# Performance work log

Hardware: AMD Instinct MI355X
Metric: run time of the kernel (lower is better)

## Reference

```python
import jax, jax.numpy as jnp
import numpy as np

B, T, C, H = 4, 4096, 1024, 64

def setup_inputs() -> dict:
    key = jax.random.key(0)
    k1, k2, k3, k4, k5 = jax.random.split(key, 5)
    scale = 0.02
    return {
        "x": jax.random.normal(k1, (B, T, C), dtype=jnp.float32),
        "head_bias": jax.random.normal(k2, (T, T), dtype=jnp.float32) * 0.1,
        "w_k": jax.random.normal(k3, (C, H), dtype=jnp.float32) * scale,
        "w_q": jax.random.normal(k4, (C, H), dtype=jnp.float32) * scale,
        "w_v": jax.random.normal(k5, (C, H), dtype=jnp.float32) * scale,
    }

def reference(x, head_bias, w_k, w_q, w_v):
    # x: (B,T,C) ; projections: (B,T,H)
    k = jnp.einsum('btc,ch->bth', x, w_k)
    q = jnp.einsum('btc,ch->bth', x, w_q)
    v = jnp.einsum('btc,ch->bth', x, w_v)
    Tq = x.shape[1]
    # scores: (B,T,T) with RPE bias and causal mask
    scores = jnp.einsum('bqh,bkh->bqk', q, k) * (k.shape[-1] ** -0.5)
    scores = scores + head_bias[None, :, :]
    causal = jnp.tril(jnp.ones((Tq, Tq), dtype=bool))
    scores = jnp.where(causal[None, :, :], scores, -jnp.inf)
    weights = jax.nn.softmax(scores, axis=-1)
    out = jnp.einsum('bqk,bkh->bqh', weights, v)
    return out
```

## Files before the change

kernel.cpp:

```cpp
#include <hip/hip_runtime.h>
#include <hip/hip_bf16.h>


#define T_DIM 4096
#define C_DIM 1024
#define CK    256

typedef __attribute__((ext_vector_type(8))) short s16x8;
typedef __attribute__((ext_vector_type(4))) float f32x4;
typedef __attribute__((ext_vector_type(2))) unsigned int u32x2;
typedef __attribute__((ext_vector_type(4))) unsigned int u32x4;

__device__ __forceinline__ short f2bf(float f) {
    unsigned u = __builtin_bit_cast(unsigned, f);
    u += 0x7FFFu + ((u >> 16) & 1u);
    return (short)(u >> 16);
}
__device__ __forceinline__ unsigned pack2(float a, float b) {
    unsigned ua = __builtin_bit_cast(unsigned, a);
    unsigned ub = __builtin_bit_cast(unsigned, b);
    ua += 0x7FFFu + ((ua >> 16) & 1u);
    ub += 0x7FFFu + ((ub >> 16) & 1u);
    return __builtin_amdgcn_perm(ub, ua, 0x07060302u);
}
__device__ __forceinline__ float bf2f(short s) {
    unsigned u = ((unsigned)(unsigned short)s) << 16;
    return __builtin_bit_cast(float, u);
}
__device__ __forceinline__ int chunk_off(int qt) {
    int g = qt >> 4, r = qt & 15;
    return qt + 8 * g * (g - 1) + r * g;
}

__global__ __launch_bounds__(256) void prep_frag(
    const float* __restrict__ wk, const float* __restrict__ wq,
    const float* __restrict__ wv, short* __restrict__ wfrag)
{
    int ksAll = blockIdx.x, mat = blockIdx.y;
    const float* w = (mat == 0) ? wk : ((mat == 1) ? wq : wv);
    float sc = (mat == 1) ? 0.125f : 1.0f;
    int nt = threadIdx.x >> 6, lane = threadIdx.x & 63;
    int quad = lane >> 4, l15 = lane & 15;
    int h = nt * 16 + l15;
    int cb = ksAll * 32 + quad * 8;
    s16x8 v;
    #pragma unroll
    for (int j = 0; j < 8; ++j) v[j] = f2bf(w[(cb + j) * 64 + h] * sc);
    *(s16x8*)&wfrag[((ksAll * 12 + mat * 4 + nt) * 64 + lane) * 8] = v;
}

union ProjSmem {
    short xs[32][1032];
    struct {
        short comb[2][16][136];
        short vsep[64][40];
    } c;
};

__global__ __launch_bounds__(256, 2) void proj_fused(
    const float* __restrict__ x, const short* __restrict__ wfrag,
    short* __restrict__ qb, short* __restrict__ kfrag, short* __restrict__ vfrag)
{
    __shared__ __align__(16) ProjSmem sm;

    int tid = threadIdx.x;
    int w = tid >> 6, lane = tid & 63;
    int rt = w >> 1, h = w & 1;
    int l15 = lane & 15, quad = lane >> 4;
    int m0 = blockIdx.x * 32;

    s16x8 fA[12], fB[12];
    {
        const s16x8* fb = (const s16x8*)&wfrag[((size_t)(h * 16) * 12 * 64 + lane) * 8];
        #pragma unroll
        for (int f = 0; f < 12; ++f) fA[f] = fb[f * 64];
    }

    #pragma unroll 8
    for (int p = 0; p < 32; ++p) {
        f32x4 v = *(const f32x4*)&x[(size_t)(m0 + p) * C_DIM + tid * 4];
        u32x2 d;
        d[0] = pack2(v[0], v[1]);
        d[1] = pack2(v[2], v[3]);
        *(u32x2*)&sm.xs[p][tid * 4] = d;
    }
    __syncthreads();

    f32x4 acc[12];
    #pragma unroll
    for (int i = 0; i < 12; ++i) acc[i] = (f32x4){0.f, 0.f, 0.f, 0.f};

    #pragma unroll 1
    for (int ks = 0; ks < 16; ks += 2) {
        {
            const s16x8* fb = (const s16x8*)&wfrag[((size_t)(h * 16 + ks + 1) * 12 * 64 + lane) * 8];
            #pragma unroll
            for (int f = 0; f < 12; ++f) fB[f] = fb[f * 64];
        }
        s16x8 af = *(const s16x8*)&sm.xs[rt * 16 + l15][(h * 16 + ks) * 32 + quad * 8];
        #pragma unroll
        for (int f = 0; f < 12; ++f)
            acc[f] = __builtin_amdgcn_mfma_f32_16x16x32_bf16(af, fA[f], acc[f], 0, 0, 0);
        if (ks + 2 < 16) {
            const s16x8* fb = (const s16x8*)&wfrag[((size_t)(h * 16 + ks + 2) * 12 * 64 + lane) * 8];
            #pragma unroll
            for (int f = 0; f < 12; ++f) fA[f] = fb[f * 64];
        }
        s16x8 af2 = *(const s16x8*)&sm.xs[rt * 16 + l15][(h * 16 + ks + 1) * 32 + quad * 8];
        #pragma unroll
        for (int f = 0; f < 12; ++f)
            acc[f] = __builtin_amdgcn_mfma_f32_16x16x32_bf16(af2, fB[f], acc[f], 0, 0, 0);
    }
    __syncthreads();

    if (h == 1) {
        #pragma unroll
        for (int f = 0; f < 8; ++f)
            #pragma unroll
            for (int r = 0; r < 4; ++r)
                sm.c.comb[rt][quad * 4 + r][(f >> 2) * 64 + (f & 3) * 16 + l15] = f2bf(acc[f][r]);
        #pragma unroll
        for (int f = 8; f < 12; ++f)
            #pragma unroll
            for (int r = 0; r < 4; ++r)
                sm.c.vsep[(f & 3) * 16 + l15][rt * 16 + quad * 4 + r] = f2bf(acc[f][r]);
    }
    __syncthreads();
    if (h == 0) {
        #pragma unroll
        for (int f = 0; f < 8; ++f)
            #pragma unroll
            for (int r = 0; r < 4; ++r) {
                int col = (f >> 2) * 64 + (f & 3) * 16 + l15, rr = quad * 4 + r;
                sm.c.comb[rt][rr][col] = f2bf(acc[f][r] + bf2f(sm.c.comb[rt][rr][col]));
            }
        #pragma unroll
        for (int f = 8; f < 12; ++f)
            #pragma unroll
            for (int r = 0; r < 4; ++r) {
                int hh = (f & 3) * 16 + l15, kk = rt * 16 + quad * 4 + r;
                sm.c.vsep[hh][kk] = f2bf(acc[f][r] + bf2f(sm.c.vsep[hh][kk]));
            }
    }
    __syncthreads();

    int b = m0 >> 12, t0 = m0 & 4095;
    int t016 = t0 >> 4, kt32 = t0 >> 5;
    {
        int row = tid >> 3, ch = tid & 7;
        s16x8 v = *(const s16x8*)&sm.c.comb[row >> 4][row & 15][64 + ch * 8];
        *(s16x8*)&qb[(size_t)(m0 + row) * 64 + ch * 8] = v;
    }
    {
        int kt = w & 1, ks = w >> 1;
        s16x8 v = *(const s16x8*)&sm.c.comb[kt][l15][ks * 32 + quad * 8];
        *(s16x8*)&kfrag[(size_t)(((b * 256 + t016 + kt) * 2 + ks) * 64 + lane) * 8] = v;
    }
    {
        int nt = w;
        s16x8 v = *(const s16x8*)&sm.c.vsep[nt * 16 + l15][quad * 8];
        *(s16x8*)&vfrag[(size_t)(((b * 128 + kt32) * 4 + nt) * 64 + lane) * 8] = v;
    }
}

#define ALOAD4(A0, A1, A2, A3, AD) do {                                       \
    asm volatile("global_load_dwordx4 %0, %1, off"                            \
                 : "=&v"(A0) : "v"(AD));                                      \
    asm volatile("global_load_dwordx4 %0, %1, off offset:1024"                \
                 : "=&v"(A1) : "v"(AD));                                      \
    asm volatile("global_load_dwordx4 %0, %1, off offset:2048"                \
                 : "=&v"(A2) : "v"(AD));                                      \
    asm volatile("global_load_dwordx4 %0, %1, off offset:3072"                \
                 : "=&v"(A3) : "v"(AD));                                      \
} while (0)

#define WAITV8() do { asm volatile("s_waitcnt vmcnt(8)");                     \
                      __builtin_amdgcn_sched_barrier(0); } while (0)
#define WAITV0() do { asm volatile("s_waitcnt vmcnt(0)");                     \
                      __builtin_amdgcn_sched_barrier(0); } while (0)

#define SOFT(N, AS, KL, RO, Q0S, LS, PLO, PHI) do {                           \
    f32x4 _vb = *(const f32x4*)&blds[(RO) + l15][(KL) + (N) * 16 + quad * 4]; \
    float _sv[4];                                                             \
    _Pragma("unroll")                                                         \
    for (int _r = 0; _r < 4; ++_r) {                                          \
        _sv[_r] = (AS)[_r] + _vb[_r];                                         \
        if (mask_on && (kabs + (N) * 16 + quad * 4 + _r > (Q0S) + l15))       \
            _sv[_r] = -__builtin_inff();                                      \
        float _p = __expf(_sv[_r]);                                           \
        _sv[_r] = _p;                                                         \
        LS += _p;                                                             \
    }                                                                         \
    PLO = pack2(_sv[0], _sv[1]);                                              \
    PHI = pack2(_sv[2], _sv[3]);                                              \
} while (0)

#define PERM4(P0, P1, P2, P3)                                                 \
    asm("v_permlane32_swap_b32 %0, %1" : "+v"(P0), "+v"(P2));                 \
    asm("v_permlane16_swap_b32 %0, %1" : "+v"(P0), "+v"(P2));                 \
    asm("v_permlane32_swap_b32 %0, %1" : "+v"(P1), "+v"(P3));                 \
    asm("v_permlane16_swap_b32 %0, %1" : "+v"(P1), "+v"(P3));

#define COMPUTEK(AK, BV, k0) do {                                             \
    int _kl = (k0) - kstart;                                                  \
    int kabs = (k0);                                                          \
    f32x4 _aS0 = (f32x4){0.f, 0.f, 0.f, 0.f};                                 \
    f32x4 _aS1 = (f32x4){0.f, 0.f, 0.f, 0.f};                                 \
    f32x4 _aS2 = (f32x4){0.f, 0.f, 0.f, 0.f};                                 \
    f32x4 _aS3 = (f32x4){0.f, 0.f, 0.f, 0.f};                                 \
    _aS0 = __builtin_amdgcn_mfma_f32_16x16x32_bf16(AK[0], aq0, _aS0, 0, 0, 0); \
    _aS0 = __builtin_amdgcn_mfma_f32_16x16x32_bf16(AK[1], aq1, _aS0, 0, 0, 0); \
    _aS1 = __builtin_amdgcn_mfma_f32_16x16x32_bf16(AK[2], aq0, _aS1, 0, 0, 0); \
    _aS1 = __builtin_amdgcn_mfma_f32_16x16x32_bf16(AK[3], aq1, _aS1, 0, 0, 0); \
    _aS2 = __builtin_amdgcn_mfma_f32_16x16x32_bf16(AK[0], aq2, _aS2, 0, 0, 0); \
    _aS2 = __builtin_amdgcn_mfma_f32_16x16x32_bf16(AK[1], aq3, _aS2, 0, 0, 0); \
    _aS3 = __builtin_amdgcn_mfma_f32_16x16x32_bf16(AK[2], aq2, _aS3, 0, 0, 0); \
    _aS3 = __builtin_amdgcn_mfma_f32_16x16x32_bf16(AK[3], aq3, _aS3, 0, 0, 0); \
    unsigned _p0, _p1, _p2, _p3, _p4, _p5, _p6, _p7;                          \
    SOFT(0, _aS0, _kl, 0, q0, l_sum0, _p0, _p1);                              \
    SOFT(1, _aS1, _kl, 0, q0, l_sum0, _p2, _p3);                              \
    SOFT(0, _aS2, _kl, 16, q0 + 16, l_sum1, _p4, _p5);                        \
    SOFT(1, _aS3, _kl, 16, q0 + 16, l_sum1, _p6, _p7);                        \
    PERM4(_p0, _p1, _p2, _p3);                                                \
    PERM4(_p4, _p5, _p6, _p7);                                                \
    u32x4 _apuA = (u32x4){_p0, _p1, _p2, _p3};                                \
    u32x4 _apuB = (u32x4){_p4, _p5, _p6, _p7};                                \
    s16x8 _apA = __builtin_bit_cast(s16x8, _apuA);                            \
    s16x8 _apB = __builtin_bit_cast(s16x8, _apuB);                            \
    _Pragma("unroll")                                                         \
    for (int _n = 0; _n < 4; ++_n) {                                          \
        accO[_n]     = __builtin_amdgcn_mfma_f32_16x16x32_bf16(_apA, BV[_n], accO[_n],     0, 0, 0); \
        accO[_n + 4] = __builtin_amdgcn_mfma_f32_16x16x32_bf16(_apB, BV[_n], accO[_n + 4], 0, 0, 0); \
    }                                                                         \
} while (0)

__global__ __launch_bounds__(256, 3) void flash_part(
    const short* __restrict__ qb, const short* __restrict__ kfrag,
    const short* __restrict__ vfrag, const float* __restrict__ bias,
    short* __restrict__ po)
{
    int g = blockIdx.x, c = blockIdx.y;
    if (c > (g >> 3)) return;
    int q0 = g * 32;
    int kstart = c * CK;
    int kend = min(kstart + CK, q0 + 32);

    __shared__ __align__(16) float blds[32][269];

    int w = threadIdx.x >> 6, lane = threadIdx.x & 63;
    int b = w;
    int l15 = lane & 15, quad = lane >> 4;

    #pragma unroll
    for (int p = 0; p < 8; ++p)
        *(f32x4*)&blds[p * 4 + w][lane * 4] =
            *(const f32x4*)&bias[(size_t)(q0 + p * 4 + w) * T_DIM + kstart + lane * 4];

    const short* qrow = qb + (size_t)(b * T_DIM + q0 + l15) * 64;
    s16x8 aq0 = *(const s16x8*)(qrow + quad * 8);
    s16x8 aq1 = *(const s16x8*)(qrow + 32 + quad * 8);
    const short* qrow2 = qrow + 16 * 64;
    s16x8 aq2 = *(const s16x8*)(qrow2 + quad * 8);
    s16x8 aq3 = *(const s16x8*)(qrow2 + 32 + quad * 8);

    float l_sum0 = 0.f, l_sum1 = 0.f;
    f32x4 accO[8];
    #pragma unroll
    for (int nt = 0; nt < 8; ++nt) accO[nt] = (f32x4){0.f, 0.f, 0.f, 0.f};

    const short* kfb = kfrag + (size_t)b * 256 * 2 * 512;
    const short* vfb = vfrag + (size_t)b * 128 * 4 * 512;
    bool mask_on = (kend > q0);

    __syncthreads();

    const char* kadd = (const char*)kfb + (size_t)kstart * 128 + lane * 16;
    const char* vadd = (const char*)vfb + (size_t)kstart * 128 + lane * 16;
    s16x8 akA[4], akB[4], bvA[4], bvB[4];
    ALOAD4(akA[0], akA[1], akA[2], akA[3], kadd);
    ALOAD4(bvA[0], bvA[1], bvA[2], bvA[3], vadd);

    int nk = kend - kstart;
    int krel = 0;
    while (true) {
        bool more = (krel + 32 < nk);
        if (more) {
            const char* ka = kadd + (size_t)(krel + 32) * 128;
            const char* va = vadd + (size_t)(krel + 32) * 128;
            ALOAD4(akB[0], akB[1], akB[2], akB[3], ka);
            ALOAD4(bvB[0], bvB[1], bvB[2], bvB[3], va);
            WAITV8();
        } else {
            WAITV0();
        }
        COMPUTEK(akA, bvA, kstart + krel);
        if (!more) break;
        krel += 32;
        bool more2 = (krel + 32 < nk);
        if (more2) {
            const char* ka = kadd + (size_t)(krel + 32) * 128;
            const char* va = vadd + (size_t)(krel + 32) * 128;
            ALOAD4(akA[0], akA[1], akA[2], akA[3], ka);
            ALOAD4(bvA[0], bvA[1], bvA[2], bvA[3], va);
            WAITV8();
        } else {
            WAITV0();
        }
        COMPUTEK(akB, bvB, kstart + krel);
        if (!more2) break;
        krel += 32;
    }

    l_sum0 += __shfl_xor(l_sum0, 16, 64);
    l_sum0 += __shfl_xor(l_sum0, 32, 64);
    l_sum1 += __shfl_xor(l_sum1, 16, 64);
    l_sum1 += __shfl_xor(l_sum1, 32, 64);

    short* baseA = po + (size_t)((chunk_off(g * 2) + c) * 4 + b) * 1040;
    #pragma unroll
    for (int nt = 0; nt < 4; ++nt)
        #pragma unroll
        for (int r = 0; r < 4; ++r)
            baseA[(quad * 4 + r) * 64 + nt * 16 + l15] = f2bf(accO[nt][r]);
    if (quad == 0) baseA[1024 + l15] = f2bf(l_sum0);

    short* baseB = po + (size_t)((chunk_off(g * 2 + 1) + c) * 4 + b) * 1040;
    #pragma unroll
    for (int nt = 0; nt < 4; ++nt)
        #pragma unroll
        for (int r = 0; r < 4; ++r)
            baseB[(quad * 4 + r) * 64 + nt * 16 + l15] = f2bf(accO[nt + 4][r]);
    if (quad == 0) baseB[1024 + l15] = f2bf(l_sum1);
}

__global__ __launch_bounds__(256) void flash_reduce(
    const short* __restrict__ po, float* __restrict__ out)
{
    int idx = blockIdx.x * 256 + threadIdx.x;
    int row = idx >> 3, c8 = idx & 7;
    int b = row >> 12, t = row & 4095;
    int qt = t >> 4, rloc = t & 15;
    int nc = (t >> 8) + 1;
    int off = chunk_off(qt);
    float o[8];
    #pragma unroll
    for (int j = 0; j < 8; ++j) o[j] = 0.f;
    float l = 0.f;
    #pragma unroll 1
    for (int cc = 0; cc < nc; ++cc) {
        const short* base = po + (size_t)((off + cc) * 4 + b) * 1040;
        s16x8 v = *(const s16x8*)&base[rloc * 64 + c8 * 8];
        #pragma unroll
        for (int j = 0; j < 8; ++j) o[j] += bf2f(v[j]);
        l += bf2f(base[1024 + rloc]);
    }
    float inv = 1.0f / l;
    f32x4 r0 = (f32x4){o[0] * inv, o[1] * inv, o[2] * inv, o[3] * inv};
    f32x4 r1 = (f32x4){o[4] * inv, o[5] * inv, o[6] * inv, o[7] * inv};
    float* op = &out[(size_t)row * 64 + c8 * 8];
    *(f32x4*)op = r0;
    *(f32x4*)(op + 4) = r1;
}

extern "C" void kernel_launch(void* const* d_in, const int* in_sizes, int n_in,
                              void* d_out, int out_size, void* d_ws, size_t ws_size,
                              hipStream_t stream) {
    (void)in_sizes; (void)n_in; (void)out_size; (void)ws_size;
    const float* x    = (const float*)d_in[0];
    const float* bias = (const float*)d_in[1];
    const float* wk   = (const float*)d_in[2];
    const float* wq   = (const float*)d_in[3];
    const float* wv   = (const float*)d_in[4];
    float* out = (float*)d_out;

    short* wfrag = (short*)d_ws;
    short* qb    = wfrag + 196608;
    short* kfrag = qb + 1048576;
    short* vfrag = kfrag + 1048576;
    short* po    = vfrag + 1048576;

    prep_frag<<<dim3(32, 3), dim3(256), 0, stream>>>(wk, wq, wv, wfrag);
    proj_fused<<<dim3(512), dim3(256), 0, stream>>>(x, wfrag, qb, kfrag, vfrag);
    flash_part<<<dim3(128, 16), dim3(256), 0, stream>>>(qb, kfrag, vfrag, bias, po);
    flash_reduce<<<dim3(512), dim3(256), 0, stream>>>(po, out);
}
```

Before: 193.5 us.

## Split projection K-reduction across four waves per row tile with fp32 LDS combine

The projection kernel now launches 512 threads per block, so each 16-row tile splits the C=1024 reduction across four waves instead of two. Partial sums are combined in fp32 shared memory through a serialized three-step accumulation rather than bf16 round-trips. The final bf16 conversion happens on write-out, with output work spread over eight waves. This aims to add latency hiding and parallelism to the projection stage, at the cost of more syncs, more LDS traffic and higher register pressure under launch_bounds(512,4).

```diff
diff --git a/kernel.cpp b/kernel.cpp
--- a/kernel.cpp
+++ b/kernel.cpp
@@ -31,6 +31,22 @@
     int g = qt >> 4, r = qt & 15;
     return qt + 8 * g * (g - 1) + r * g;
 }
+
+#define ALOAD4(A0, A1, A2, A3, AD) do {                                       \
+    asm volatile("global_load_dwordx4 %0, %1, off"                            \
+                 : "=&v"(A0) : "v"(AD));                                      \
+    asm volatile("global_load_dwordx4 %0, %1, off offset:1024"                \
+                 : "=&v"(A1) : "v"(AD));                                      \
+    asm volatile("global_load_dwordx4 %0, %1, off offset:2048"                \
+                 : "=&v"(A2) : "v"(AD));                                      \
+    asm volatile("global_load_dwordx4 %0, %1, off offset:3072"                \
+                 : "=&v"(A3) : "v"(AD));                                      \
+} while (0)
+
+#define WAITV8()  do { asm volatile("s_waitcnt vmcnt(8)");                    \
+                       __builtin_amdgcn_sched_barrier(0); } while (0)
+#define WAITV0()  do { asm volatile("s_waitcnt vmcnt(0)");                    \
+                       __builtin_amdgcn_sched_barrier(0); } while (0)
 
 __global__ __launch_bounds__(256) void prep_frag(
     const float* __restrict__ wk, const float* __restrict__ wq,
@@ -52,12 +68,12 @@
 union ProjSmem {
     short xs[32][1032];
     struct {
-        short comb[2][16][136];
-        short vsep[64][40];
+        float comb[2][16][140];
+        float vsep[64][44];
     } c;
 };
 
-__global__ __launch_bounds__(256, 2) void proj_fused(
+__global__ __launch_bounds__(512, 4) void proj_fused(
     const float* __restrict__ x, const short* __restrict__ wfrag,
     short* __restrict__ qb, short* __restrict__ kfrag, short* __restrict__ vfrag)
 {
@@ -65,24 +81,26 @@
 
     int tid = threadIdx.x;
     int w = tid >> 6, lane = tid & 63;
-    int rt = w >> 1, h = w & 1;
+    int rt = w >> 2, h = w & 3;
     int l15 = lane & 15, quad = lane >> 4;
     int m0 = blockIdx.x * 32;
 
     s16x8 fA[12], fB[12];
     {
-        const s16x8* fb = (const s16x8*)&wfrag[((size_t)(h * 16) * 12 * 64 + lane) * 8];
+        const s16x8* fb = (const s16x8*)&wfrag[((size_t)(h * 8) * 12 * 64 + lane) * 8];
         #pragma unroll
         for (int f = 0; f < 12; ++f) fA[f] = fb[f * 64];
     }
 
     #pragma unroll 8
-    for (int p = 0; p < 32; ++p) {
-        f32x4 v = *(const f32x4*)&x[(size_t)(m0 + p) * C_DIM + tid * 4];
+    for (int p = 0; p < 16; ++p) {
+        int prow = p * 2 + (tid >> 8);
+        int pcol = (tid & 255) * 4;
+        f32x4 v = *(const f32x4*)&x[(size_t)(m0 + prow) * C_DIM + pcol];
         u32x2 d;
         d[0] = pack2(v[0], v[1]);
         d[1] = pack2(v[2], v[3]);
-        *(u32x2*)&sm.xs[p][tid * 4] = d;
+        *(u32x2*)&sm.xs[prow][pcol] = d;
     }
     __syncthreads();
 
@@ -91,93 +109,98 @@
     for (int i = 0; i < 12; ++i) acc[i] = (f32x4){0.f, 0.f, 0.f, 0.f};
 
     #pragma unroll 1
-    for (int ks = 0; ks < 16; ks += 2) {
+    for (int ks = 0; ks < 8; ks += 2) {
         {
-            const s16x8* fb = (const s16x8*)&wfrag[((size_t)(h * 16 + ks + 1) * 12 * 64 + lane) * 8];
+            const s16x8* fb = (const s16x8*)&wfrag[((size_t)(h * 8 + ks + 1) * 12 * 64 + lane) * 8];
             #pragma unroll
             for (int f = 0; f < 12; ++f) fB[f] = fb[f * 64];
         }
-        s16x8 af = *(const s16x8*)&sm.xs[rt * 16 + l15][(h * 16 + ks) * 32 + quad * 8];
+        s16x8 af = *(const s16x8*)&sm.xs[rt * 16 + l15][(h * 8 + ks) * 32 + quad * 8];
         #pragma unroll
         for (int f = 0; f < 12; ++f)
             acc[f] = __builtin_amdgcn_mfma_f32_16x16x32_bf16(af, fA[f], acc[f], 0, 0, 0);
-        if (ks + 2 < 16) {
-            const s16x8* fb = (const s16x8*)&wfrag[((size_t)(h * 16 + ks + 2) * 12 * 64 + lane) * 8];
+        if (ks + 2 < 8) {
+            const s16x8* fb = (const s16x8*)&wfrag[((size_t)(h * 8 + ks + 2) * 12 * 64 + lane) * 8];
             #pragma unroll
             for (int f = 0; f < 12; ++f) fA[f] = fb[f * 64];
         }
-        s16x8 af2 = *(const s16x8*)&sm.xs[rt * 16 + l15][(h * 16 + ks + 1) * 32 + quad * 8];
+        s16x8 af2 = *(const s16x8*)&sm.xs[rt * 16 + l15][(h * 8 + ks + 1) * 32 + quad * 8];
         #pragma unroll
         for (int f = 0; f < 12; ++f)
             acc[f] = __builtin_amdgcn_mfma_f32_16x16x32_bf16(af2, fB[f], acc[f], 0, 0, 0);
     }
     __syncthreads();
 
-    if (h == 1) {
+    if (h == 3) {
         #pragma unroll
         for (int f = 0; f < 8; ++f)
             #pragma unroll
             for (int r = 0; r < 4; ++r)
-                sm.c.comb[rt][quad * 4 + r][(f >> 2) * 64 + (f & 3) * 16 + l15] = f2bf(acc[f][r]);
+                sm.c.comb[rt][quad * 4 + r][(f >> 2) * 64 + (f & 3) * 16 + l15] = acc[f][r];
         #pragma unroll
         for (int f = 8; f < 12; ++f)
             #pragma unroll
             for (int r = 0; r < 4; ++r)
-                sm.c.vsep[(f & 3) * 16 + l15][rt * 16 + quad * 4 + r] = f2bf(acc[f][r]);
+                sm.c.vsep[(f & 3) * 16 + l15][rt * 16 + quad * 4 + r] = acc[f][r];
     }
     __syncthreads();
-    if (h == 0) {
-        #pragma unroll
-        for (int f = 0; f < 8; ++f)
-            #pragma unroll
-            for (int r = 0; r < 4; ++r) {
-                int col = (f >> 2) * 64 + (f & 3) * 16 + l15, rr = quad * 4 + r;
-                sm.c.comb[rt][rr][col] = f2bf(acc[f][r] + bf2f(sm.c.comb[rt][rr][col]));
-            }
-        #pragma unroll
-        for (int f = 8; f < 12; ++f)
-            #pragma unroll
-            for (int r = 0; r < 4; ++r) {
-                int hh = (f & 3) * 16 + l15, kk = rt * 16 + quad * 4 + r;
-                sm.c.vsep[hh][kk] = f2bf(acc[f][r] + bf2f(sm.c.vsep[hh][kk]));
-            }
-    }
-    __syncthreads();
+    #pragma unroll 1
+    for (int hs = 2; hs >= 0; --hs) {
+        if (h == hs) {
+            #pragma unroll
+            for (int f = 0; f < 8; ++f)
+                #pragma unroll
+                for (int r = 0; r < 4; ++r)
+                    sm.c.comb[rt][quad * 4 + r][(f >> 2) * 64 + (f & 3) * 16 + l15] += acc[f][r];
+            #pragma unroll
+            for (int f = 8; f < 12; ++f)
+                #pragma unroll
+                for (int r = 0; r < 4; ++r)
+                    sm.c.vsep[(f & 3) * 16 + l15][rt * 16 + quad * 4 + r] += acc[f][r];
+        }
+        __syncthreads();
+    }
 
     int b = m0 >> 12, t0 = m0 & 4095;
     int t016 = t0 >> 4, kt32 = t0 >> 5;
-    {
-        int row = tid >> 3, ch = tid & 7;
-        s16x8 v = *(const s16x8*)&sm.c.comb[row >> 4][row & 15][64 + ch * 8];
-        *(s16x8*)&qb[(size_t)(m0 + row) * 64 + ch * 8] = v;
-    }
-    {
-        int kt = w & 1, ks = w >> 1;
-        s16x8 v = *(const s16x8*)&sm.c.comb[kt][l15][ks * 32 + quad * 8];
-        *(s16x8*)&kfrag[(size_t)(((b * 256 + t016 + kt) * 2 + ks) * 64 + lane) * 8] = v;
-    }
-    {
-        int nt = w;
-        s16x8 v = *(const s16x8*)&sm.c.vsep[nt * 16 + l15][quad * 8];
-        *(s16x8*)&vfrag[(size_t)(((b * 128 + kt32) * 4 + nt) * 64 + lane) * 8] = v;
-    }
-}
-
-#define ALOAD4(A0, A1, A2, A3, AD) do {                                       \
-    asm volatile("global_load_dwordx4 %0, %1, off"                            \
-                 : "=&v"(A0) : "v"(AD));                                      \
-    asm volatile("global_load_dwordx4 %0, %1, off offset:1024"                \
-                 : "=&v"(A1) : "v"(AD));                                      \
-    asm volatile("global_load_dwordx4 %0, %1, off offset:2048"                \
-                 : "=&v"(A2) : "v"(AD));                                      \
-    asm volatile("global_load_dwordx4 %0, %1, off offset:3072"                \
-                 : "=&v"(A3) : "v"(AD));                                      \
-} while (0)
-
-#define WAITV8() do { asm volatile("s_waitcnt vmcnt(8)");                     \
-                      __builtin_amdgcn_sched_barrier(0); } while (0)
-#define WAITV0() do { asm volatile("s_waitcnt vmcnt(0)");                     \
-                      __builtin_amdgcn_sched_barrier(0); } while (0)
+    if (w < 4) {
+        {
+            int row = tid >> 3, ch = tid & 7;
+            const float* pa = &sm.c.comb[row >> 4][row & 15][64 + ch * 8];
+            f32x4 a0 = *(const f32x4*)pa, a1 = *(const f32x4*)(pa + 4);
+            s16x8 v;
+            #pragma unroll
+            for (int j = 0; j < 4; ++j) {
+                v[j]     = f2bf(a0[j]);
+                v[j + 4] = f2bf(a1[j]);
+            }
+            *(s16x8*)&qb[(size_t)(m0 + row) * 64 + ch * 8] = v;
+        }
+        {
+            int nt = w;
+            const float* pa = &sm.c.vsep[nt * 16 + l15][quad * 8];
+            f32x4 a0 = *(const f32x4*)pa, a1 = *(const f32x4*)(pa + 4);
+            s16x8 v;
+            #pragma unroll
+            for (int j = 0; j < 4; ++j) {
+                v[j]     = f2bf(a0[j]);
+                v[j + 4] = f2bf(a1[j]);
+            }
+            *(s16x8*)&vfrag[(size_t)(((b * 128 + kt32) * 4 + nt) * 64 + lane) * 8] = v;
+        }
+    } else {
+        int w2 = w - 4, kt = w2 & 1, ks2 = w2 >> 1;
+        const float* pa = &sm.c.comb[kt][l15][ks2 * 32 + quad * 8];
+        f32x4 a0 = *(const f32x4*)pa, a1 = *(const f32x4*)(pa + 4);
+        s16x8 v;
+        #pragma unroll
+        for (int j = 0; j < 4; ++j) {
+            v[j]     = f2bf(a0[j]);
+            v[j + 4] = f2bf(a1[j]);
+        }
+        *(s16x8*)&kfrag[(size_t)(((b * 256 + t016 + kt) * 2 + ks2) * 64 + lane) * 8] = v;
+    }
+}
 
 #define SOFT(N, AS, KL, RO, Q0S, LS, PLO, PHI) do {                           \
     f32x4 _vb = *(const f32x4*)&blds[(RO) + l15][(KL) + (N) * 16 + quad * 4]; \
@@ -380,7 +403,7 @@
     short* po    = vfrag + 1048576;
 
     prep_frag<<<dim3(32, 3), dim3(256), 0, stream>>>(wk, wq, wv, wfrag);
-    proj_fused<<<dim3(512), dim3(256), 0, stream>>>(x, wfrag, qb, kfrag, vfrag);
+    proj_fused<<<dim3(512), dim3(512), 0, stream>>>(x, wfrag, qb, kfrag, vfrag);
     flash_part<<<dim3(128, 16), dim3(256), 0, stream>>>(qb, kfrag, vfrag, bias, po);
     flash_reduce<<<dim3(512), dim3(256), 0, stream>>>(po, out);
 }
```

Result: slower. 225.3 us (+16.4%).
